# Performance work log

Hardware: AMD Instinct MI355X
Metric: run time of the kernel (lower is better)

## Reference

```python
import jax, jax.numpy as jnp
import numpy as np

VEC_SIZE = 1024
N_HEADS = 16
HEAD_SIZE = VEC_SIZE // N_HEADS


def setup_inputs() -> dict:
    key = jax.random.key(0)
    k1, k2, k3 = jax.random.split(key, 3)
    x = jax.random.normal(k1, (4, 2048, VEC_SIZE), dtype=jnp.float32)
    # nn.Linear weights stored as [out, in]; we apply as x @ W.T, so store transposed [in, out]
    w_qkv = jax.random.normal(k2, (VEC_SIZE, 3 * VEC_SIZE), dtype=jnp.float32) * (1.0 / np.sqrt(VEC_SIZE))
    w_out = jax.random.normal(k3, (VEC_SIZE, VEC_SIZE), dtype=jnp.float32) * (1.0 / np.sqrt(VEC_SIZE))
    return {"x": x, "w_qkv": w_qkv, "w_out": w_out}


def reference(x, w_qkv, w_out):
    batch, seq_len, _ = x.shape
    qkv = x @ w_qkv                                   # [B, S, 3*D]
    q, k, v = jnp.split(qkv, 3, axis=-1)
    def heads(m):
        return m.reshape(batch, seq_len, N_HEADS, HEAD_SIZE).transpose(0, 2, 1, 3)  # [B,H,S,d]
    q, k, v = heads(q), heads(k), heads(v)
    scale = 1.0 / np.sqrt(HEAD_SIZE).astype(np.float32)
    scores = jnp.einsum('bhqd,bhkd->bhqk', q, k) * scale        # [B,H,S,S]
    causal = jnp.tril(jnp.ones((seq_len, seq_len), dtype=bool))
    scores = jnp.where(causal[None, None], scores, jnp.finfo(scores.dtype).min)
    probs = jax.nn.softmax(scores, axis=-1)
    attn = jnp.einsum('bhqk,bhkd->bhqd', probs, v)              # [B,H,S,d]
    attn = attn.transpose(0, 2, 1, 3).reshape(batch, seq_len, VEC_SIZE)
    return attn @ w_out
```

## Files before the change

kernel.cpp:

```cpp
#include <hip/hip_runtime.h>
#include <float.h>


#define SEQ   2048
#define DIM   1024
#define NH    16
#define HD    64
#define MROWS 8192
#define BHTOT 64

#define PREP_CAST_BLOCKS  8192
#define PREP_WQKV_BLOCKS  3072
#define PREP_WOUT_BLOCKS  1024

typedef __bf16 bf16_t;
typedef __bf16 bf16x4 __attribute__((ext_vector_type(4)));
typedef __bf16 bf16x8 __attribute__((ext_vector_type(8)));
typedef float  f32x4  __attribute__((ext_vector_type(4)));

typedef const __attribute__((address_space(1))) unsigned int* gas_ptr;
typedef __attribute__((address_space(3))) unsigned int* las_ptr;

__device__ __forceinline__ void gll16(const bf16_t* g, bf16_t* l) {
    __builtin_amdgcn_global_load_lds((gas_ptr)g, (las_ptr)l, 16, 0, 0);
}

__global__ __launch_bounds__(256) void prep_kernel(
    const float* __restrict__ x,     bf16_t* __restrict__ xb,
    const float* __restrict__ w_qkv, bf16_t* __restrict__ wqkvT,
    const float* __restrict__ w_out, bf16_t* __restrict__ woutT)
{
    __shared__ float t[32][33];
    const int blk = blockIdx.x;

    if (blk < PREP_CAST_BLOCKS) {
        int i = (blk * 256 + threadIdx.x) * 4;
        float4 v = *(const float4*)(x + i);
        bf16x4 o = { (bf16_t)v.x, (bf16_t)v.y, (bf16_t)v.z, (bf16_t)v.w };
        *(bf16x4*)(xb + i) = o;
        return;
    }

    const float* w;  bf16_t* wT;  int N, tile;
    if (blk < PREP_CAST_BLOCKS + PREP_WQKV_BLOCKS) {
        tile = blk - PREP_CAST_BLOCKS;  w = w_qkv;  wT = wqkvT;  N = 3 * DIM;
    } else {
        tile = blk - PREP_CAST_BLOCKS - PREP_WQKV_BLOCKS;  w = w_out;  wT = woutT;  N = DIM;
    }
    const int bk = (tile & 31) * 32;
    const int bn = (tile >> 5) * 32;
    const int r = threadIdx.x >> 5, c = threadIdx.x & 31;
    #pragma unroll
    for (int i = 0; i < 4; i++)
        t[r + i * 8][c] = w[(size_t)(bk + r + i * 8) * N + bn + c];
    __syncthreads();
    #pragma unroll
    for (int i = 0; i < 4; i++)
        wT[(size_t)(bn + r + i * 8) * DIM + bk + c] = (bf16_t)t[c][r + i * 8];
}

__device__ __forceinline__ void gemm_dbuf_compute(
    const bf16_t* __restrict__ Ag, const bf16_t* __restrict__ Bg,
    int bm, int bn, bf16_t* As, bf16_t* Bs, f32x4 (&acc)[4][4])
{
    const int tid = threadIdx.x;
    const int lane = tid & 63, w = tid >> 6;
    const int quad = lane >> 4, l16 = lane & 15;
    const int wr = w >> 1, wc = w & 1;

    auto stage = [&](int kt, int buf) {
        const int k0 = kt * 64;
        bf16_t* Ad = As + buf * (128 * 64);
        bf16_t* Bd = Bs + buf * (128 * 64);
        #pragma unroll
        for (int p = 0; p < 4; p++) {
            int flat = p * 256 + tid;
            int row = flat >> 3, g = flat & 7, gs = g ^ (row & 7);
            gll16(Ag + (size_t)(bm + row) * DIM + k0 + gs * 8,
                  Ad + (size_t)(p * 256 + w * 64) * 8);
            gll16(Bg + (size_t)(bn + row) * DIM + k0 + gs * 8,
                  Bd + (size_t)(p * 256 + w * 64) * 8);
        }
    };

    stage(0, 0);
    __syncthreads();

    #pragma unroll 1
    for (int kt = 0; kt < 16; kt++) {
        const int cur = kt & 1;
        if (kt < 15) stage(kt + 1, cur ^ 1);
        const bf16_t* Ac = As + cur * (128 * 64);
        const bf16_t* Bc = Bs + cur * (128 * 64);
        #pragma unroll
        for (int ks = 0; ks < 2; ks++) {
            bf16x8 af[4], bfv[4];
            #pragma unroll
            for (int mt = 0; mt < 4; mt++) {
                int row = wr * 64 + mt * 16 + l16;
                int g = (ks * 4 + quad) ^ (row & 7);
                af[mt] = *(const bf16x8*)(Ac + row * 64 + g * 8);
            }
            #pragma unroll
            for (int nt = 0; nt < 4; nt++) {
                int row = wc * 64 + nt * 16 + l16;
                int g = (ks * 4 + quad) ^ (row & 7);
                bfv[nt] = *(const bf16x8*)(Bc + row * 64 + g * 8);
            }
            #pragma unroll
            for (int mt = 0; mt < 4; mt++)
                #pragma unroll
                for (int nt = 0; nt < 4; nt++)
                    acc[mt][nt] = __builtin_amdgcn_mfma_f32_16x16x32_bf16(
                        af[mt], bfv[nt], acc[mt][nt], 0, 0, 0);
        }
        __syncthreads();
    }
}

__global__ __launch_bounds__(256) void gemm_qkv_kernel(
    const bf16_t* __restrict__ Ag,
    const bf16_t* __restrict__ Bg,
    bf16_t* __restrict__ qN, bf16_t* __restrict__ kN, bf16_t* __restrict__ vT)
{
    __shared__ __align__(16) bf16_t As[2 * 128 * 64];
    __shared__ __align__(16) bf16_t Bs[2 * 128 * 64];
    const int tid = threadIdx.x;
    const int lane = tid & 63, w = tid >> 6;
    const int quad = lane >> 4, l16 = lane & 15;
    const int wr = w >> 1, wc = w & 1;
    const int bm = blockIdx.x * 128, bn = blockIdx.y * 128;

    f32x4 acc[4][4] = {};
    gemm_dbuf_compute(Ag, Bg, bm, bn, As, Bs, acc);

    const int which = bn >> 10;
    if (which == 2) {
        #pragma unroll
        for (int mt = 0; mt < 4; mt++)
            #pragma unroll
            for (int nt = 0; nt < 4; nt++) {
                int row0 = bm + wr * 64 + mt * 16 + quad * 4;
                int b = row0 >> 11, s0 = row0 & 2047;
                int col = bn + wc * 64 + nt * 16 + l16;
                int nn = col & 1023, h = nn >> 6, d = nn & 63;
                int bh = b * NH + h;
                bf16x4 vv;
                #pragma unroll
                for (int r = 0; r < 4; r++) vv[r] = (bf16_t)acc[mt][nt][r];
                *(bf16x4*)(vT + ((size_t)bh * HD + d) * SEQ + s0) = vv;
            }
    } else {
        const float qsc = (which == 0) ? 0.18033688011112042f : 1.0f;
        bf16_t* dst = (which == 0) ? qN : kN;
        #pragma unroll
        for (int mt = 0; mt < 4; mt++)
            #pragma unroll
            for (int nt = 0; nt < 4; nt++)
                #pragma unroll
                for (int r = 0; r < 4; r++) {
                    int row = bm + wr * 64 + mt * 16 + quad * 4 + r;
                    int b = row >> 11, s = row & 2047;
                    int col = bn + wc * 64 + nt * 16 + l16;
                    int nn = col & 1023, h = nn >> 6, d = nn & 63;
                    int bh = b * NH + h;
                    dst[((size_t)bh * SEQ + s) * HD + d] = (bf16_t)(acc[mt][nt][r] * qsc);
                }
    }
}

__global__ __launch_bounds__(256) void gemm_out_kernel(
    const bf16_t* __restrict__ Ag,
    const bf16_t* __restrict__ Bg,
    float* __restrict__ out)
{
    __shared__ __align__(16) bf16_t As[2 * 128 * 64];
    __shared__ __align__(16) bf16_t Bs[2 * 128 * 64];
    const int tid = threadIdx.x;
    const int lane = tid & 63, w = tid >> 6;
    const int quad = lane >> 4, l16 = lane & 15;
    const int wr = w >> 1, wc = w & 1;
    const int bm = blockIdx.x * 128, bn = blockIdx.y * 128;

    f32x4 acc[4][4] = {};
    gemm_dbuf_compute(Ag, Bg, bm, bn, As, Bs, acc);

    #pragma unroll
    for (int mt = 0; mt < 4; mt++)
        #pragma unroll
        for (int nt = 0; nt < 4; nt++)
            #pragma unroll
            for (int r = 0; r < 4; r++) {
                int row = bm + wr * 64 + mt * 16 + quad * 4 + r;
                int col = bn + wc * 64 + nt * 16 + l16;
                out[(size_t)row * DIM + col] = acc[mt][nt][r];
            }
}

__global__ __launch_bounds__(256) void attn_kernel(
    const bf16_t* __restrict__ qN, const bf16_t* __restrict__ kN,
    const bf16_t* __restrict__ vT, bf16_t* __restrict__ attnb)
{
    __shared__ __align__(16) char smem[40960];
    bf16_t* QPs = (bf16_t*)smem;
    bf16_t* Ks  = (bf16_t*)(smem + 8192);
    bf16_t* Vs  = (bf16_t*)(smem + 24576);

    const int bh = blockIdx.x;
    const int pr = blockIdx.y;
    const int tid = threadIdx.x;
    const int lane = tid & 63, w = tid >> 6;
    const int quad = lane >> 4, l16 = lane & 15;

    const bf16_t* qbase = qN + (size_t)bh * SEQ * HD;
    const bf16_t* kbase = kN + (size_t)bh * SEQ * HD;
    const bf16_t* vbase = vT + (size_t)bh * HD * SEQ;
    const int b = bh >> 4, h = bh & 15;

    auto stage_kv = [&](int kt, int buf) {
        bf16_t* Kd = Ks + buf * 4096;
        bf16_t* Vd = Vs + buf * 4096;
        #pragma unroll
        for (int p = 0; p < 2; p++) {
            int flat = p * 256 + tid;
            int row = flat >> 3, g = flat & 7;
            int gs = g ^ (row & 7);
            gll16(kbase + (size_t)(kt * 64 + row) * HD + gs * 8, Kd + (size_t)(p * 256 + w * 64) * 8);
            gll16(vbase + (size_t)row * SEQ + kt * 64 + gs * 8,  Vd + (size_t)(p * 256 + w * 64) * 8);
        }
    };

    #pragma unroll 1
    for (int phase = 0; phase < 2; phase++) {
        const int t = (phase == 0) ? pr : 31 - pr;

        __syncthreads();
        #pragma unroll
        for (int p = 0; p < 2; p++) {
            int flat = p * 256 + tid;
            int row = flat >> 3, g = flat & 7;
            int gs = g ^ (row & 7);
            gll16(qbase + (size_t)(t * 64 + row) * HD + gs * 8,
                  QPs + (size_t)(p * 256 + w * 64) * 8);
        }
        stage_kv(0, 0);
        __syncthreads();

        bf16x8 qa[2];
        #pragma unroll
        for (int ks = 0; ks < 2; ks++) {
            int row = w * 16 + l16;
            int g = (ks * 4 + quad) ^ (row & 7);
            qa[ks] = *(const bf16x8*)(QPs + row * 64 + g * 8);
        }

        f32x4 o[4] = {};
        float l_part = 0.0f;

        const int rl = w * 16 + l16;
        const int qrow = t * 64 + rl;

        for (int kt = 0; kt <= t; kt++) {
            const int cur = kt & 1;
            if (kt < t) stage_kv(kt + 1, cur ^ 1);

            const bf16_t* Kc = Ks + cur * 4096;
            const bf16_t* Vc = Vs + cur * 4096;

            f32x4 s[4] = {};
            #pragma unroll
            for (int ks = 0; ks < 2; ks++) {
                bf16x8 kb[4];
                #pragma unroll
                for (int nt = 0; nt < 4; nt++) {
                    int row = nt * 16 + l16;
                    int g = (ks * 4 + quad) ^ (row & 7);
                    kb[nt] = *(const bf16x8*)(Kc + row * 64 + g * 8);
                }
                #pragma unroll
                for (int nt = 0; nt < 4; nt++)
                    s[nt] = __builtin_amdgcn_mfma_f32_16x16x32_bf16(
                        kb[nt], qa[ks], s[nt], 0, 0, 0);
            }

            const bool maskit = (kt == t);
            #pragma unroll
            for (int nt = 0; nt < 4; nt++) {
                bf16x4 pk;
                #pragma unroll
                for (int r = 0; r < 4; r++) {
                    float pv;
                    if (maskit) {
                        int key = kt * 64 + nt * 16 + quad * 4 + r;
                        pv = (key <= qrow) ? __builtin_amdgcn_exp2f(s[nt][r]) : 0.0f;
                    } else {
                        pv = __builtin_amdgcn_exp2f(s[nt][r]);
                    }
                    l_part += pv;
                    pk[r] = (bf16_t)pv;
                }
                int gs = (nt * 2 + (quad >> 1)) ^ (rl & 7);
                *(bf16x4*)(QPs + rl * 64 + gs * 8 + (quad & 1) * 4) = pk;
            }

            #pragma unroll
            for (int ks = 0; ks < 2; ks++) {
                bf16x8 vb[4], pb;
                #pragma unroll
                for (int dt = 0; dt < 4; dt++) {
                    int row = dt * 16 + l16;
                    int g = (ks * 4 + quad) ^ (row & 7);
                    vb[dt] = *(const bf16x8*)(Vc + row * 64 + g * 8);
                }
                {
                    int g = (ks * 4 + quad) ^ (rl & 7);
                    pb = *(const bf16x8*)(QPs + rl * 64 + g * 8);
                }
                #pragma unroll
                for (int dt = 0; dt < 4; dt++)
                    o[dt] = __builtin_amdgcn_mfma_f32_16x16x32_bf16(
                        vb[dt], pb, o[dt], 0, 0, 0);
            }

            __syncthreads();
        }

        float lsum = l_part;
        lsum += __shfl_xor(lsum, 16, 64);
        lsum += __shfl_xor(lsum, 32, 64);
        float inv = 1.0f / lsum;
        const int srow = t * 64 + w * 16 + l16;
        #pragma unroll
        for (int dt = 0; dt < 4; dt++) {
            bf16x4 ov;
            #pragma unroll
            for (int r = 0; r < 4; r++) ov[r] = (bf16_t)(o[dt][r] * inv);
            *(bf16x4*)(attnb + ((size_t)(b * SEQ + srow)) * DIM + h * HD + dt * 16 + quad * 4) = ov;
        }
    }
}

extern "C" void kernel_launch(void* const* d_in, const int* in_sizes, int n_in,
                              void* d_out, int out_size, void* d_ws, size_t ws_size,
                              hipStream_t stream) {
    const float* x     = (const float*)d_in[0];
    const float* w_qkv = (const float*)d_in[1];
    const float* w_out = (const float*)d_in[2];
    float* out = (float*)d_out;

    bf16_t* xb    = (bf16_t*)d_ws;
    bf16_t* wqkvT = xb    + (size_t)MROWS * DIM;
    bf16_t* woutT = wqkvT + (size_t)3 * DIM * DIM;
    bf16_t* qNb   = woutT + (size_t)DIM * DIM;
    bf16_t* kNb   = qNb   + (size_t)BHTOT * SEQ * HD;
    bf16_t* vTb   = kNb   + (size_t)BHTOT * SEQ * HD;
    bf16_t* attnb = vTb   + (size_t)BHTOT * SEQ * HD;

    prep_kernel<<<PREP_CAST_BLOCKS + PREP_WQKV_BLOCKS + PREP_WOUT_BLOCKS, 256, 0, stream>>>(
        x, xb, w_qkv, wqkvT, w_out, woutT);
    gemm_qkv_kernel<<<dim3(MROWS / 128, 3 * DIM / 128), 256, 0, stream>>>(xb, wqkvT, qNb, kNb, vTb);
    attn_kernel<<<dim3(BHTOT, 16), 256, 0, stream>>>(qNb, kNb, vTb, attnb);
    gemm_out_kernel<<<dim3(MROWS / 128, DIM / 128), 256, 0, stream>>>(attnb, woutT, out);
}
```

Before: 228.7 us.

## Replace direct-to-LDS GEMM staging with register-prefetched two-deep software pipeline

Changes the shared GEMM main loop from global_load_lds double buffering to loading tiles into registers two iterations ahead, then writing them to LDS before compute. Precomputes global and LDS addresses once and replaces __syncthreads with a custom lgkmcnt wait plus scheduling-barrier fence. Also sets launch bounds to two blocks per CU for both GEMM kernels. This is meant to hide global latency better, at the cost of extra VGPRs and explicit LDS write instructions.

```diff
diff --git a/kernel.cpp b/kernel.cpp
--- a/kernel.cpp
+++ b/kernel.cpp
@@ -23,6 +23,13 @@
 
 __device__ __forceinline__ void gll16(const bf16_t* g, bf16_t* l) {
     __builtin_amdgcn_global_load_lds((gas_ptr)g, (las_ptr)l, 16, 0, 0);
+}
+
+__device__ __forceinline__ void pipe_barrier() {
+    asm volatile("s_waitcnt lgkmcnt(0)" ::: "memory");
+    __builtin_amdgcn_sched_barrier(0);
+    __builtin_amdgcn_s_barrier();
+    __builtin_amdgcn_sched_barrier(0);
 }
 
 __global__ __launch_bounds__(256) void prep_kernel(
@@ -59,37 +66,61 @@
         wT[(size_t)(bn + r + i * 8) * DIM + bk + c] = (bf16_t)t[c][r + i * 8];
 }
 
-__device__ __forceinline__ void gemm_dbuf_compute(
+__device__ __forceinline__ void gemm_pipe_compute(
     const bf16_t* __restrict__ Ag, const bf16_t* __restrict__ Bg,
     int bm, int bn, bf16_t* As, bf16_t* Bs, f32x4 (&acc)[4][4])
 {
     const int tid = threadIdx.x;
-    const int lane = tid & 63, w = tid >> 6;
+    const int lane = tid & 63;
     const int quad = lane >> 4, l16 = lane & 15;
+    const int w = tid >> 6;
     const int wr = w >> 1, wc = w & 1;
 
-    auto stage = [&](int kt, int buf) {
+    const bf16_t* gA[4]; const bf16_t* gB[4]; int ldsOff[4];
+    #pragma unroll
+    for (int p = 0; p < 4; p++) {
+        int flat = p * 256 + tid;
+        int row = flat >> 3, g = flat & 7, gs = g ^ (row & 7);
+        gA[p] = Ag + (size_t)(bm + row) * DIM + gs * 8;
+        gB[p] = Bg + (size_t)(bn + row) * DIM + gs * 8;
+        ldsOff[p] = flat * 8;
+    }
+
+    bf16x8 a0[4], b0[4], a1[4], b1[4];
+
+    auto loadT = [&](int kt, bf16x8 (&ra)[4], bf16x8 (&rb)[4]) {
         const int k0 = kt * 64;
+        #pragma unroll
+        for (int p = 0; p < 4; p++) {
+            ra[p] = *(const bf16x8*)(gA[p] + k0);
+            rb[p] = *(const bf16x8*)(gB[p] + k0);
+        }
+    };
+    auto writeT = [&](int buf, bf16x8 (&ra)[4], bf16x8 (&rb)[4]) {
         bf16_t* Ad = As + buf * (128 * 64);
         bf16_t* Bd = Bs + buf * (128 * 64);
         #pragma unroll
         for (int p = 0; p < 4; p++) {
-            int flat = p * 256 + tid;
-            int row = flat >> 3, g = flat & 7, gs = g ^ (row & 7);
-            gll16(Ag + (size_t)(bm + row) * DIM + k0 + gs * 8,
-                  Ad + (size_t)(p * 256 + w * 64) * 8);
-            gll16(Bg + (size_t)(bn + row) * DIM + k0 + gs * 8,
-                  Bd + (size_t)(p * 256 + w * 64) * 8);
+            *(bf16x8*)(Ad + ldsOff[p]) = ra[p];
+            *(bf16x8*)(Bd + ldsOff[p]) = rb[p];
         }
     };
 
-    stage(0, 0);
-    __syncthreads();
-
-    #pragma unroll 1
+    loadT(0, a0, b0);
+    loadT(1, a1, b1);
+    writeT(0, a0, b0);
+    pipe_barrier();
+
+    #pragma unroll 2
     for (int kt = 0; kt < 16; kt++) {
         const int cur = kt & 1;
-        if (kt < 15) stage(kt + 1, cur ^ 1);
+        if ((kt & 1) == 0) {
+            if (kt + 2 < 16) loadT(kt + 2, a0, b0);
+            writeT(1, a1, b1);
+        } else {
+            if (kt + 2 < 16) loadT(kt + 2, a1, b1);
+            if (kt + 1 < 16) writeT(0, a0, b0);
+        }
         const bf16_t* Ac = As + cur * (128 * 64);
         const bf16_t* Bc = Bs + cur * (128 * 64);
         #pragma unroll
@@ -114,11 +145,11 @@
                     acc[mt][nt] = __builtin_amdgcn_mfma_f32_16x16x32_bf16(
                         af[mt], bfv[nt], acc[mt][nt], 0, 0, 0);
         }
-        __syncthreads();
-    }
-}
-
-__global__ __launch_bounds__(256) void gemm_qkv_kernel(
+        pipe_barrier();
+    }
+}
+
+__global__ __launch_bounds__(256, 2) void gemm_qkv_kernel(
     const bf16_t* __restrict__ Ag,
     const bf16_t* __restrict__ Bg,
     bf16_t* __restrict__ qN, bf16_t* __restrict__ kN, bf16_t* __restrict__ vT)
@@ -132,7 +163,7 @@
     const int bm = blockIdx.x * 128, bn = blockIdx.y * 128;
 
     f32x4 acc[4][4] = {};
-    gemm_dbuf_compute(Ag, Bg, bm, bn, As, Bs, acc);
+    gemm_pipe_compute(Ag, Bg, bm, bn, As, Bs, acc);
 
     const int which = bn >> 10;
     if (which == 2) {
@@ -169,7 +200,7 @@
     }
 }
 
-__global__ __launch_bounds__(256) void gemm_out_kernel(
+__global__ __launch_bounds__(256, 2) void gemm_out_kernel(
     const bf16_t* __restrict__ Ag,
     const bf16_t* __restrict__ Bg,
     float* __restrict__ out)
@@ -183,7 +214,7 @@
     const int bm = blockIdx.x * 128, bn = blockIdx.y * 128;
 
     f32x4 acc[4][4] = {};
-    gemm_dbuf_compute(Ag, Bg, bm, bn, As, Bs, acc);
+    gemm_pipe_compute(Ag, Bg, bm, bn, As, Bs, acc);
 
     #pragma unroll
     for (int mt = 0; mt < 4; mt++)
```

Measured after the change: 233.3 us. No clear change (+2.0%).
